# Optimization experiments

Hardware: AMD Instinct MI355X
Metric: run time of the kernel (lower is better)

## Reference

```python
import jax, jax.numpy as jnp
import numpy as np

BLOCK_SIZE_KV = 16
SCALE = 0.08838834764831845  # 1/sqrt(128)


def setup_inputs() -> dict:
    key = jax.random.key(0)
    k0, k1, k2, k3, k4 = jax.random.split(key, 5)
    B, H, D, KVH = 32, 32, 128, 8
    MAX_BLOCKS = 256                 # 4096-token max context / 16-token pages
    N_PHYS_BLOCKS = B * MAX_BLOCKS   # 8192 physical pages
    q = jax.random.normal(k0, (B, H, D), jnp.float32)
    k_cache = jax.random.normal(k1, (N_PHYS_BLOCKS, BLOCK_SIZE_KV, KVH, D), jnp.float32)
    v_cache = jax.random.normal(k2, (N_PHYS_BLOCKS, BLOCK_SIZE_KV, KVH, D), jnp.float32)
    # each logical page maps to a distinct physical page (vLLM-style allocation)
    block_tables = jax.random.permutation(k3, N_PHYS_BLOCKS).reshape(B, MAX_BLOCKS).astype(jnp.int32)
    context_lens = jax.random.randint(k4, (B,), 1, MAX_BLOCKS * BLOCK_SIZE_KV + 1, jnp.int32)
    return {"q": q, "k_cache": k_cache, "v_cache": v_cache,
            "block_tables": block_tables, "context_lens": context_lens}


def reference(q, k_cache, v_cache, block_tables, context_lens):
    # q: [B, H, D]; k/v_cache: [NB, 16, KVH, D]; block_tables: [B, MB]; context_lens: [B]
    B, H, D = q.shape
    KVH = k_cache.shape[2]
    G = H // KVH                                  # GQA group size
    MB = block_tables.shape[1]
    S = MB * BLOCK_SIZE_KV                        # max logical context
    # gather paged KV per sequence: [B, MB, 16, KVH, D] -> [B, S, KVH, D]
    K = k_cache[block_tables].reshape(B, S, KVH, D)
    V = v_cache[block_tables].reshape(B, S, KVH, D)
    qg = q.reshape(B, KVH, G, D)
    scores = jnp.einsum('bkgd,bskd->bkgs', qg, K) * jnp.float32(SCALE)
    valid = (jnp.arange(S)[None, :] < context_lens[:, None])  # [B, S]
    scores = jnp.where(valid[:, None, None, :], scores, -jnp.inf)
    p = jax.nn.softmax(scores, axis=-1)           # online-softmax equivalent
    out = jnp.einsum('bkgs,bskd->bkgd', p, V).reshape(B, H, D)
    return out
```

## Files before the change

kernel.cpp:

```cpp
#include <hip/hip_runtime.h>


constexpr int Dh   = 128;
constexpr int Gq   = 4;
constexpr int KVH  = 8;
constexpr int Hq   = 32;
constexpr int Bb   = 32;
constexpr int MB   = 256;
constexpr int PAGE = 16;
constexpr float SCALE = 0.08838834764831845f;

constexpr int NPARTS      = 64;
constexpr int PART_TOKENS = 64;
constexpr int PG_FLOATS   = PAGE * KVH * Dh;
constexpr int ROW_FLOATS  = KVH * Dh;

constexpr int PART_STRIDE = Hq * Dh + 2 * Hq;

struct QuadR { float4 k[4], v[4]; };

__global__ __launch_bounds__(256, 3)
void attn_partial(const float* __restrict__ q,
                  const float* __restrict__ kc,
                  const float* __restrict__ vc,
                  const int*   __restrict__ bt,
                  const int*   __restrict__ cl,
                  float*       __restrict__ ws)
{
    const int part = blockIdx.x & (NPARTS - 1);
    const int b    = blockIdx.x >> 6;

    const int ctx    = cl[b];
    const int pstart = part * PART_TOKENS;
    if (pstart >= ctx) return;
    const int n  = min(PART_TOKENS, ctx - pstart);
    const int TC = (n + 3) >> 2;

    const int t      = threadIdx.x;
    const int kvh    = t >> 5;
    const int lane32 = t & 31;
    const int doff   = lane32 * 4;
    const int t4     = t * 4;

    const int4 pg = *(const int4*)(bt + b * MB + (pstart >> 4));

    float4 qv[Gq];
    {
        const float* qbase = q + (size_t)(b * Hq + kvh * Gq) * Dh + doff;
        #pragma unroll
        for (int g = 0; g < Gq; ++g) {
            float4 x = *(const float4*)(qbase + g * Dh);
            qv[g] = make_float4(x.x * SCALE, x.y * SCALE, x.z * SCALE, x.w * SCALE);
        }
    }

    float4 acc[Gq];
    float  m_run[Gq], l_run[Gq];
    #pragma unroll
    for (int g = 0; g < Gq; ++g) {
        acc[g] = make_float4(0.f, 0.f, 0.f, 0.f);
        m_run[g] = -1e30f;
        l_run[g] = 0.f;
    }

    auto physof = [&](int c) -> int {
        const int p = c >> 2;
        return p == 0 ? pg.x : (p == 1 ? pg.y : (p == 2 ? pg.z : pg.w));
    };

    auto LOADQ = [&](QuadR& H, int c) {
        const size_t off = (size_t)physof(c) * PG_FLOATS
                         + (size_t)((c & 3) * 4) * ROW_FLOATS + t4;
        const float* kp = kc + off;
        const float* vp = vc + off;
        #pragma unroll
        for (int j = 0; j < 4; ++j) {
            H.k[j] = *(const float4*)(kp + j * ROW_FLOATS);
            H.v[j] = *(const float4*)(vp + j * ROW_FLOATS);
        }
    };

    auto COMPUTEQ = [&](const QuadR& H, int c) {
        const int tb = c * 4;
        float s[4][Gq];
        #pragma unroll
        for (int j = 0; j < 4; ++j) {
            const bool vj = (tb + j) < n;
            #pragma unroll
            for (int g = 0; g < Gq; ++g) {
                float d = H.k[j].x * qv[g].x + H.k[j].y * qv[g].y
                        + H.k[j].z * qv[g].z + H.k[j].w * qv[g].w;
                d += __shfl_xor(d, 1);
                d += __shfl_xor(d, 2);
                d += __shfl_xor(d, 4);
                d += __shfl_xor(d, 8);
                d += __shfl_xor(d, 16);
                s[j][g] = vj ? d : -1e30f;
            }
        }
        #pragma unroll
        for (int g = 0; g < Gq; ++g) {
            const float tm = fmaxf(fmaxf(s[0][g], s[1][g]), fmaxf(s[2][g], s[3][g]));
            const float mn    = fmaxf(m_run[g], tm);
            const float alpha = __expf(m_run[g] - mn);
            m_run[g] = mn;
            const float p0 = __expf(s[0][g] - mn);
            const float p1 = __expf(s[1][g] - mn);
            const float p2 = __expf(s[2][g] - mn);
            const float p3 = __expf(s[3][g] - mn);
            l_run[g] = l_run[g] * alpha + (p0 + p1 + p2 + p3);
            acc[g].x = fmaf(p3, H.v[3].x, fmaf(p2, H.v[2].x,
                       fmaf(p1, H.v[1].x, fmaf(p0, H.v[0].x, acc[g].x * alpha))));
            acc[g].y = fmaf(p3, H.v[3].y, fmaf(p2, H.v[2].y,
                       fmaf(p1, H.v[1].y, fmaf(p0, H.v[0].y, acc[g].y * alpha))));
            acc[g].z = fmaf(p3, H.v[3].z, fmaf(p2, H.v[2].z,
                       fmaf(p1, H.v[1].z, fmaf(p0, H.v[0].z, acc[g].z * alpha))));
            acc[g].w = fmaf(p3, H.v[3].w, fmaf(p2, H.v[2].w,
                       fmaf(p1, H.v[1].w, fmaf(p0, H.v[0].w, acc[g].w * alpha))));
        }
    };

    QuadR A, B;
    LOADQ(A, 0);
    int c = 0;
    while (true) {
        if (c + 1 < TC) LOADQ(B, c + 1);
        COMPUTEQ(A, c);
        ++c; if (c >= TC) break;
        if (c + 1 < TC) LOADQ(A, c + 1);
        COMPUTEQ(B, c);
        ++c; if (c >= TC) break;
    }

    float* wp = ws + (size_t)(b * NPARTS + part) * PART_STRIDE;
    #pragma unroll
    for (int g = 0; g < Gq; ++g)
        *(float4*)(wp + (kvh * Gq + g) * Dh + doff) = acc[g];
    if (lane32 == 0) {
        #pragma unroll
        for (int g = 0; g < Gq; ++g) {
            wp[Hq * Dh + kvh * Gq + g]      = m_run[g];
            wp[Hq * Dh + Hq + kvh * Gq + g] = l_run[g];
        }
    }
}

__global__ __launch_bounds__(256, 4)
void attn_reduce(const float* __restrict__ ws,
                 const int*   __restrict__ cl,
                 float*       __restrict__ out)
{
    const int b       = blockIdx.x >> 2;
    const int quarter = blockIdx.x & 3;
    const int tid     = threadIdx.x;
    const int h       = quarter * 8 + (tid >> 5);
    const int doff    = (tid & 31) * 4;

    const int ctx = cl[b];
    const int np  = min(NPARTS, (ctx + PART_TOKENS - 1) / PART_TOKENS);

    const float* base = ws + (size_t)b * NPARTS * PART_STRIDE;

    float m = -1e30f;
    for (int p = 0; p < np; ++p)
        m = fmaxf(m, base[p * PART_STRIDE + Hq * Dh + h]);

    float L = 0.f;
    float ax = 0.f, ay = 0.f, az = 0.f, aw = 0.f;
    for (int p = 0; p < np; ++p) {
        const float* bp = base + p * PART_STRIDE;
        const float c = __expf(bp[Hq * Dh + h] - m);
        L += bp[Hq * Dh + Hq + h] * c;
        const float4 v = *(const float4*)(bp + h * Dh + doff);
        ax = fmaf(c, v.x, ax);
        ay = fmaf(c, v.y, ay);
        az = fmaf(c, v.z, az);
        aw = fmaf(c, v.w, aw);
    }
    const float inv = 1.f / L;
    float* op = out + (size_t)(b * Hq + h) * Dh + doff;
    *(float4*)op = make_float4(ax * inv, ay * inv, az * inv, aw * inv);
}

extern "C" void kernel_launch(void* const* d_in, const int* in_sizes, int n_in,
                              void* d_out, int out_size, void* d_ws, size_t ws_size,
                              hipStream_t stream) {
    const float* q  = (const float*)d_in[0];
    const float* kc = (const float*)d_in[1];
    const float* vc = (const float*)d_in[2];
    const int*   bt = (const int*)d_in[3];
    const int*   cl = (const int*)d_in[4];
    float* out = (float*)d_out;
    float* ws  = (float*)d_ws;

    attn_partial<<<dim3(Bb * NPARTS), dim3(256), 0, stream>>>(q, kc, vc, bt, cl, ws);
    attn_reduce<<<dim3(Bb * 4), dim3(256), 0, stream>>>(ws, cl, out);
}
```

Baseline: 149.5 us.

## Warp-specialize partial attention with producer DMA-to-LDS and persistent blocks

Rewrites the partial kernel as a persistent 512-block grid in which four producer waves stream K/V rows into a double-buffered LDS ring using global_load_lds, and four consumer waves run the online softmax from LDS. Handoff between the two groups uses LDS flag counters and spin-waits instead of block barriers. The aim is to keep more bytes in flight and hide memory latency behind compute in this bandwidth-bound decode. In exchange, half the threads do no arithmetic, spin-wait overhead is added, and the hand-written waitcnt and flag ordering could race if the LDS writes are not visible when the flags are bumped.

```diff
diff --git a/kernel.cpp b/kernel.cpp
--- a/kernel.cpp
+++ b/kernel.cpp
@@ -14,12 +14,18 @@
 constexpr int PART_TOKENS = 64;
 constexpr int PG_FLOATS   = PAGE * KVH * Dh;
 constexpr int ROW_FLOATS  = KVH * Dh;
+constexpr int NUNITS      = Bb * NPARTS;
+constexpr int NBLOCKS     = 512;
 
 constexpr int PART_STRIDE = Hq * Dh + 2 * Hq;
 
-struct QuadR { float4 k[4], v[4]; };
-
-__global__ __launch_bounds__(256, 3)
+__device__ __forceinline__ void gld16(const float* g, float* l) {
+    __builtin_amdgcn_global_load_lds(
+        (const __attribute__((address_space(1))) void*)g,
+        (__attribute__((address_space(3))) void*)l, 16, 0, 0);
+}
+
+__global__ __launch_bounds__(512, 4)
 void attn_partial(const float* __restrict__ q,
                   const float* __restrict__ kc,
                   const float* __restrict__ vc,
@@ -27,120 +33,154 @@
                   const int*   __restrict__ cl,
                   float*       __restrict__ ws)
 {
-    const int part = blockIdx.x & (NPARTS - 1);
-    const int b    = blockIdx.x >> 6;
-
-    const int ctx    = cl[b];
-    const int pstart = part * PART_TOKENS;
-    if (pstart >= ctx) return;
-    const int n  = min(PART_TOKENS, ctx - pstart);
-    const int TC = (n + 3) >> 2;
+    __shared__ float kv[2][2][4][1024];
+    __shared__ int flags[4];
+    volatile int* vf = flags;
 
     const int t      = threadIdx.x;
-    const int kvh    = t >> 5;
-    const int lane32 = t & 31;
+    const int wv     = t >> 6;
+    const int lane   = t & 63;
+    const bool prod  = (wv >= 4);
+    const int pw     = wv - 4;
+    const int lane32 = lane & 31;
+    const int kvh    = (wv << 1) | (lane >> 5);
     const int doff   = lane32 * 4;
-    const int t4     = t * 4;
-
-    const int4 pg = *(const int4*)(bt + b * MB + (pstart >> 4));
-
-    float4 qv[Gq];
-    {
-        const float* qbase = q + (size_t)(b * Hq + kvh * Gq) * Dh + doff;
-        #pragma unroll
-        for (int g = 0; g < Gq; ++g) {
-            float4 x = *(const float4*)(qbase + g * Dh);
-            qv[g] = make_float4(x.x * SCALE, x.y * SCALE, x.z * SCALE, x.w * SCALE);
-        }
-    }
-
-    float4 acc[Gq];
-    float  m_run[Gq], l_run[Gq];
-    #pragma unroll
-    for (int g = 0; g < Gq; ++g) {
-        acc[g] = make_float4(0.f, 0.f, 0.f, 0.f);
-        m_run[g] = -1e30f;
-        l_run[g] = 0.f;
-    }
-
-    auto physof = [&](int c) -> int {
-        const int p = c >> 2;
-        return p == 0 ? pg.x : (p == 1 ? pg.y : (p == 2 ? pg.z : pg.w));
-    };
-
-    auto LOADQ = [&](QuadR& H, int c) {
-        const size_t off = (size_t)physof(c) * PG_FLOATS
-                         + (size_t)((c & 3) * 4) * ROW_FLOATS + t4;
-        const float* kp = kc + off;
-        const float* vp = vc + off;
-        #pragma unroll
-        for (int j = 0; j < 4; ++j) {
-            H.k[j] = *(const float4*)(kp + j * ROW_FLOATS);
-            H.v[j] = *(const float4*)(vp + j * ROW_FLOATS);
-        }
-    };
-
-    auto COMPUTEQ = [&](const QuadR& H, int c) {
-        const int tb = c * 4;
-        float s[4][Gq];
-        #pragma unroll
-        for (int j = 0; j < 4; ++j) {
-            const bool vj = (tb + j) < n;
+
+    for (int u = blockIdx.x; u < NUNITS; u += NBLOCKS) {
+        const int b    = u & (Bb - 1);
+        const int part = u >> 5;
+
+        const int ctx    = cl[b];
+        const int pstart = part * PART_TOKENS;
+        if (pstart >= ctx) continue;
+        const int n   = min(PART_TOKENS, ctx - pstart);
+        const int NCH = (n + 3) >> 2;
+
+        __syncthreads();
+        if (t < 4) flags[t] = 0;
+        __syncthreads();
+
+        const int4 pg = *(const int4*)(bt + b * MB + (pstart >> 4));
+        auto physof = [&](int pi) -> int {
+            return pi == 0 ? pg.x : (pi == 1 ? pg.y : (pi == 2 ? pg.z : pg.w));
+        };
+
+        if (prod) {
+            auto ISSUE = [&](int c) {
+                const int tok  = c * 4 + pw;
+                const int phys = physof(tok >> 4);
+                const size_t base = (size_t)phys * PG_FLOATS
+                                  + (size_t)(tok & 15) * ROW_FLOATS + lane * 4;
+                const int s = c & 1;
+                float* kd = &kv[s][0][pw][0];
+                float* vd = &kv[s][1][pw][0];
+                #pragma unroll
+                for (int i = 0; i < 4; ++i) gld16(kc + base + i * 256, kd + i * 256);
+                #pragma unroll
+                for (int i = 0; i < 4; ++i) gld16(vc + base + i * 256, vd + i * 256);
+            };
+
+            ISSUE(0);
+            for (int c = 0; c < NCH; ++c) {
+                if (c + 1 < NCH) {
+                    const int s1 = (c + 1) & 1;
+                    if (c + 1 >= 2) {
+                        const int tgt = 4 * ((c + 1) >> 1);
+                        while (vf[2 + s1] < tgt) __builtin_amdgcn_s_sleep(2);
+                    }
+                    ISSUE(c + 1);
+                    asm volatile("s_waitcnt vmcnt(8)" ::: "memory");
+                } else {
+                    asm volatile("s_waitcnt vmcnt(0)" ::: "memory");
+                }
+                if (lane == 0) atomicAdd((int*)&flags[c & 1], 1);
+            }
+        } else {
+            float4 qv[Gq];
+            {
+                const float* qbase = q + (size_t)(b * Hq + kvh * Gq) * Dh + doff;
+                #pragma unroll
+                for (int g = 0; g < Gq; ++g) {
+                    float4 x = *(const float4*)(qbase + g * Dh);
+                    qv[g] = make_float4(x.x * SCALE, x.y * SCALE,
+                                        x.z * SCALE, x.w * SCALE);
+                }
+            }
+            float4 acc[Gq];
+            float  m_run[Gq], l_run[Gq];
             #pragma unroll
             for (int g = 0; g < Gq; ++g) {
-                float d = H.k[j].x * qv[g].x + H.k[j].y * qv[g].y
-                        + H.k[j].z * qv[g].z + H.k[j].w * qv[g].w;
-                d += __shfl_xor(d, 1);
-                d += __shfl_xor(d, 2);
-                d += __shfl_xor(d, 4);
-                d += __shfl_xor(d, 8);
-                d += __shfl_xor(d, 16);
-                s[j][g] = vj ? d : -1e30f;
-            }
-        }
-        #pragma unroll
-        for (int g = 0; g < Gq; ++g) {
-            const float tm = fmaxf(fmaxf(s[0][g], s[1][g]), fmaxf(s[2][g], s[3][g]));
-            const float mn    = fmaxf(m_run[g], tm);
-            const float alpha = __expf(m_run[g] - mn);
-            m_run[g] = mn;
-            const float p0 = __expf(s[0][g] - mn);
-            const float p1 = __expf(s[1][g] - mn);
-            const float p2 = __expf(s[2][g] - mn);
-            const float p3 = __expf(s[3][g] - mn);
-            l_run[g] = l_run[g] * alpha + (p0 + p1 + p2 + p3);
-            acc[g].x = fmaf(p3, H.v[3].x, fmaf(p2, H.v[2].x,
-                       fmaf(p1, H.v[1].x, fmaf(p0, H.v[0].x, acc[g].x * alpha))));
-            acc[g].y = fmaf(p3, H.v[3].y, fmaf(p2, H.v[2].y,
-                       fmaf(p1, H.v[1].y, fmaf(p0, H.v[0].y, acc[g].y * alpha))));
-            acc[g].z = fmaf(p3, H.v[3].z, fmaf(p2, H.v[2].z,
-                       fmaf(p1, H.v[1].z, fmaf(p0, H.v[0].z, acc[g].z * alpha))));
-            acc[g].w = fmaf(p3, H.v[3].w, fmaf(p2, H.v[2].w,
-                       fmaf(p1, H.v[1].w, fmaf(p0, H.v[0].w, acc[g].w * alpha))));
-        }
-    };
-
-    QuadR A, B;
-    LOADQ(A, 0);
-    int c = 0;
-    while (true) {
-        if (c + 1 < TC) LOADQ(B, c + 1);
-        COMPUTEQ(A, c);
-        ++c; if (c >= TC) break;
-        if (c + 1 < TC) LOADQ(A, c + 1);
-        COMPUTEQ(B, c);
-        ++c; if (c >= TC) break;
-    }
-
-    float* wp = ws + (size_t)(b * NPARTS + part) * PART_STRIDE;
-    #pragma unroll
-    for (int g = 0; g < Gq; ++g)
-        *(float4*)(wp + (kvh * Gq + g) * Dh + doff) = acc[g];
-    if (lane32 == 0) {
-        #pragma unroll
-        for (int g = 0; g < Gq; ++g) {
-            wp[Hq * Dh + kvh * Gq + g]      = m_run[g];
-            wp[Hq * Dh + Hq + kvh * Gq + g] = l_run[g];
+                acc[g] = make_float4(0.f, 0.f, 0.f, 0.f);
+                m_run[g] = -1e30f;
+                l_run[g] = 0.f;
+            }
+
+            for (int c = 0; c < NCH; ++c) {
+                const int s   = c & 1;
+                const int tgt = 4 * ((c >> 1) + 1);
+                while (vf[s] < tgt) __builtin_amdgcn_s_sleep(2);
+
+                float4 kk[4], vv[4];
+                #pragma unroll
+                for (int j = 0; j < 4; ++j) {
+                    kk[j] = *(const float4*)&kv[s][0][j][kvh * 128 + doff];
+                    vv[j] = *(const float4*)&kv[s][1][j][kvh * 128 + doff];
+                }
+
+                const int tb = c * 4;
+                float sc[4][Gq];
+                #pragma unroll
+                for (int j = 0; j < 4; ++j) {
+                    const bool vj = (tb + j) < n;
+                    #pragma unroll
+                    for (int g = 0; g < Gq; ++g) {
+                        float d = kk[j].x * qv[g].x + kk[j].y * qv[g].y
+                                + kk[j].z * qv[g].z + kk[j].w * qv[g].w;
+                        d += __shfl_xor(d, 1);
+                        d += __shfl_xor(d, 2);
+                        d += __shfl_xor(d, 4);
+                        d += __shfl_xor(d, 8);
+                        d += __shfl_xor(d, 16);
+                        sc[j][g] = vj ? d : -1e30f;
+                    }
+                }
+                #pragma unroll
+                for (int g = 0; g < Gq; ++g) {
+                    const float tm = fmaxf(fmaxf(sc[0][g], sc[1][g]),
+                                           fmaxf(sc[2][g], sc[3][g]));
+                    const float mn    = fmaxf(m_run[g], tm);
+                    const float alpha = __expf(m_run[g] - mn);
+                    m_run[g] = mn;
+                    const float p0 = __expf(sc[0][g] - mn);
+                    const float p1 = __expf(sc[1][g] - mn);
+                    const float p2 = __expf(sc[2][g] - mn);
+                    const float p3 = __expf(sc[3][g] - mn);
+                    l_run[g] = l_run[g] * alpha + (p0 + p1 + p2 + p3);
+                    acc[g].x = fmaf(p3, vv[3].x, fmaf(p2, vv[2].x,
+                               fmaf(p1, vv[1].x, fmaf(p0, vv[0].x, acc[g].x * alpha))));
+                    acc[g].y = fmaf(p3, vv[3].y, fmaf(p2, vv[2].y,
+                               fmaf(p1, vv[1].y, fmaf(p0, vv[0].y, acc[g].y * alpha))));
+                    acc[g].z = fmaf(p3, vv[3].z, fmaf(p2, vv[2].z,
+                               fmaf(p1, vv[1].z, fmaf(p0, vv[0].z, acc[g].z * alpha))));
+                    acc[g].w = fmaf(p3, vv[3].w, fmaf(p2, vv[2].w,
+                               fmaf(p1, vv[1].w, fmaf(p0, vv[0].w, acc[g].w * alpha))));
+                }
+
+                asm volatile("" ::: "memory");
+                if (lane == 0) atomicAdd((int*)&flags[2 + s], 1);
+            }
+
+            float* wp = ws + (size_t)(b * NPARTS + part) * PART_STRIDE;
+            #pragma unroll
+            for (int g = 0; g < Gq; ++g)
+                *(float4*)(wp + (kvh * Gq + g) * Dh + doff) = acc[g];
+            if (lane32 == 0) {
+                #pragma unroll
+                for (int g = 0; g < Gq; ++g) {
+                    wp[Hq * Dh + kvh * Gq + g]      = m_run[g];
+                    wp[Hq * Dh + Hq + kvh * Gq + g] = l_run[g];
+                }
+            }
         }
     }
 }
@@ -193,6 +233,6 @@
     float* out = (float*)d_out;
     float* ws  = (float*)d_ws;
 
-    attn_partial<<<dim3(Bb * NPARTS), dim3(256), 0, stream>>>(q, kc, vc, bt, cl, ws);
+    attn_partial<<<dim3(NBLOCKS), dim3(512), 0, stream>>>(q, kc, vc, bt, cl, ws);
     attn_reduce<<<dim3(Bb * 4), dim3(256), 0, stream>>>(ws, cl, out);
 }
```

Result: slower. 245.4 us (+64.1%).
